# Kernel tuning notes

Hardware: AMD Instinct MI355X
Metric: run time of the kernel (lower is better)

Reference implementation:

```python
import jax, jax.numpy as jnp
import numpy as np

N_NODES = 100000
N_EDGES = 1600000
D_IN = 128
D_HID = 128
D_OUT = 64


def setup_inputs() -> dict:
    key = jax.random.key(0)
    ks = jax.random.split(key, 8)
    x = jax.random.normal(ks[0], (N_NODES, D_IN), dtype=jnp.float32)
    edge_index = jax.random.randint(ks[1], (2, N_EDGES), 0, N_NODES, dtype=jnp.int64)
    s1 = 1.0 / np.sqrt(D_IN)
    s2 = 1.0 / np.sqrt(D_HID)
    W1 = jax.random.uniform(ks[2], (D_IN, D_HID), jnp.float32, -s1, s1)
    b1 = jnp.zeros((D_HID,), jnp.float32)
    W2 = jax.random.uniform(ks[3], (D_HID, D_HID), jnp.float32, -s2, s2)
    b2 = jnp.zeros((D_HID,), jnp.float32)
    fc_W = jax.random.uniform(ks[4], (D_HID, D_OUT), jnp.float32, -s2, s2)
    fc_b = jax.random.uniform(ks[5], (D_OUT,), jnp.float32, -s2, s2)
    return {"x": x, "edge_index": edge_index, "W1": W1, "b1": b1,
            "W2": W2, "b2": b2, "fc_W": fc_W, "fc_b": fc_b}


def _gcn_norm(edge_index, n_nodes):
    # add self-loops, compute symmetric normalization D^{-1/2} A D^{-1/2}
    loops = jnp.arange(n_nodes, dtype=edge_index.dtype)
    src = jnp.concatenate([edge_index[0], loops])  # [E+N]
    dst = jnp.concatenate([edge_index[1], loops])
    ones = jnp.ones(src.shape[0], jnp.float32)
    deg = jax.ops.segment_sum(ones, dst, num_segments=n_nodes)  # [N]
    dinv = 1.0 / jnp.sqrt(deg)  # deg >= 1 thanks to self-loops
    norm = dinv[src] * dinv[dst]  # [E+N]
    return src, dst, norm


def _gcn_conv(x, W, b, src, dst, norm, n_nodes):
    h = x @ W                                  # [N, d]
    msg = h[src] * norm[:, None]               # gather + scale, [E+N, d]
    out = jax.ops.segment_sum(msg, dst, num_segments=n_nodes)  # scatter-add
    return out + b


def reference(x, edge_index, W1, b1, W2, b2, fc_W, fc_b):
    n = x.shape[0]
    src, dst, norm = _gcn_norm(edge_index, n)
    h = jax.nn.relu(_gcn_conv(x, W1, b1, src, dst, norm, n))
    # dropout is identity in inference mode
    h = jax.nn.relu(_gcn_conv(h, W2, b2, src, dst, norm, n))
    return h @ fc_W + fc_b
```

## Files before the change

kernel.cpp:

```cpp
#include <hip/hip_runtime.h>

typedef __attribute__((ext_vector_type(8))) short bf16x8;
typedef __attribute__((ext_vector_type(4))) float f32x4;
typedef __attribute__((ext_vector_type(2))) float f32x2;

__device__ __forceinline__ unsigned short f2bf(float x) {
  union { float f; unsigned u; } v; v.f = x;
  return (unsigned short)((v.u + 0x7fffu + ((v.u >> 16) & 1u)) >> 16);
}


__global__ __launch_bounds__(256) void bhist_k(const int* __restrict__ dst,
                                               int* __restrict__ bcnt, int E, int B) {
  __shared__ int h[512];
  for (int i = threadIdx.x; i < B; i += 256) h[i] = 0;
  __syncthreads();
  for (int e = blockIdx.x * 256 + threadIdx.x; e < E; e += gridDim.x * 256)
    atomicAdd(&h[dst[e] >> 8], 1);
  __syncthreads();
  for (int i = threadIdx.x; i < B; i += 256)
    if (h[i]) atomicAdd(&bcnt[i * 16], h[i]);
}

__global__ __launch_bounds__(256) void bin_k(const int* __restrict__ src,
                                             const int* __restrict__ dst,
                                             const int* __restrict__ bcnt,
                                             int* __restrict__ bfill,
                                             unsigned* __restrict__ ebuf, int E, int B) {
  __shared__ int hist[512];
  __shared__ int base[512];
  __shared__ int sd[256];
  int t = threadIdx.x;
  int i0 = 2 * t, i1 = 2 * t + 1;
  int v0 = (i0 < B) ? bcnt[i0 * 16] : 0;
  int v1 = (i1 < B) ? bcnt[i1 * 16] : 0;
  int ts = v0 + v1;
  sd[t] = ts; __syncthreads();
  for (int off = 1; off < 256; off <<= 1) {
    int x = (t >= off) ? sd[t - off] : 0;
    __syncthreads();
    sd[t] += x;
    __syncthreads();
  }
  int excl = sd[t] - ts;
  base[i0] = excl;
  base[i1] = excl + v0;
  __syncthreads();

  int chunk = (E + gridDim.x - 1) / gridDim.x;
  int e0 = blockIdx.x * chunk;
  int e1 = e0 + chunk; if (e1 > E) e1 = E;
  for (int i = t; i < B; i += 256) hist[i] = 0;
  __syncthreads();
  for (int e = e0 + t; e < e1; e += 256) atomicAdd(&hist[dst[e] >> 8], 1);
  __syncthreads();
  for (int i = t; i < B; i += 256) {
    int c = hist[i];
    hist[i] = base[i] + (c ? atomicAdd(&bfill[i * 16], c) : 0);
  }
  __syncthreads();
  for (int e = e0 + t; e < e1; e += 256) {
    int d = dst[e];
    int b = d >> 8;
    int pos = atomicAdd(&hist[b], 1);
    ebuf[pos] = ((unsigned)(d & 255) << 17) | (unsigned)src[e];
  }
}

__global__ __launch_bounds__(256) void bsort_k(const unsigned* __restrict__ ebuf,
                                               const int* __restrict__ bcnt,
                                               int* __restrict__ csr,
                                               int* __restrict__ row_start,
                                               float* __restrict__ dinv, int N, int B, int E) {
  __shared__ int cnt[256];
  __shared__ int sd[256];
  __shared__ int ofs[256];
  __shared__ int sorted[8192];
  __shared__ int s_bs, s_m;
  int b = blockIdx.x, t = threadIdx.x;
  int i0 = 2 * t, i1 = 2 * t + 1;
  int v0 = (i0 < B) ? bcnt[i0 * 16] : 0;
  int v1 = (i1 < B) ? bcnt[i1 * 16] : 0;
  int ts = v0 + v1;
  sd[t] = ts; __syncthreads();
  for (int off = 1; off < 256; off <<= 1) {
    int x = (t >= off) ? sd[t - off] : 0;
    __syncthreads();
    sd[t] += x;
    __syncthreads();
  }
  int excl = sd[t] - ts;
  if (i0 == b) { s_bs = excl; s_m = v0; }
  if (i1 == b) { s_bs = excl + v0; s_m = v1; }
  if (b == 0 && t == 0) row_start[N] = E;
  __syncthreads();
  int bs = s_bs, m = s_m;
  if (m > 8192) m = 8192;

  cnt[t] = 0;
  __syncthreads();
  for (int i = t; i < m; i += 256) atomicAdd(&cnt[ebuf[bs + i] >> 17], 1);
  __syncthreads();
  int deg = cnt[t];
  sd[t] = deg; __syncthreads();
  for (int off = 1; off < 256; off <<= 1) {
    int x = (t >= off) ? sd[t - off] : 0;
    __syncthreads();
    sd[t] += x;
    __syncthreads();
  }
  int nexcl = sd[t] - deg;
  ofs[t] = nexcl;
  int node = (b << 8) + t;
  if (node < N) {
    row_start[node] = bs + nexcl;
    dinv[node] = rsqrtf((float)(deg + 1));
  }
  __syncthreads();
  for (int i = t; i < m; i += 256) {
    unsigned r = ebuf[bs + i];
    int d = r >> 17;
    int p = atomicAdd(&ofs[d], 1);
    if (p < 8192) sorted[p] = (int)(r & 0x1FFFFu);
  }
  __syncthreads();
  for (int i = t; i < m; i += 256) csr[bs + i] = sorted[i];
}

template <int NCOL, bool INF32, bool OUTF32, bool SCALE>
__global__ __launch_bounds__(256) void gemm_k(const void* __restrict__ Ap,
                                              const float* __restrict__ W,
                                              const float* __restrict__ bias,
                                              const float* __restrict__ rowscale,
                                              void* __restrict__ Cp, int M) {
  __shared__ __align__(16) unsigned short Ws[NCOL * 136];
  int tid = threadIdx.x;
  for (int e = tid; e < 128 * NCOL; e += 256) {
    int k = e / NCOL, n = e % NCOL;
    Ws[n * 136 + k] = f2bf(W[e]);
  }
  __syncthreads();

  int wave = tid >> 6, lane = tid & 63;
  int q = lane >> 4, r = lane & 15;
  const int NT = NCOL / 16;
  int ntile = M >> 4;
  for (int tile = blockIdx.x * 4 + wave; tile < ntile; tile += gridDim.x * 4) {
    int row = tile * 16 + r;
    bf16x8 a[4];
    if (INF32) {
      const float* A = (const float*)Ap + (size_t)row * 128 + q * 8;
#pragma unroll
      for (int kk = 0; kk < 4; kk++) {
        const float4* p = (const float4*)(A + kk * 32);
        float4 f0 = p[0], f1 = p[1];
        bf16x8 tt;
        tt[0] = (short)f2bf(f0.x); tt[1] = (short)f2bf(f0.y);
        tt[2] = (short)f2bf(f0.z); tt[3] = (short)f2bf(f0.w);
        tt[4] = (short)f2bf(f1.x); tt[5] = (short)f2bf(f1.y);
        tt[6] = (short)f2bf(f1.z); tt[7] = (short)f2bf(f1.w);
        a[kk] = tt;
      }
    } else {
      const unsigned short* A = (const unsigned short*)Ap + (size_t)row * 128 + q * 8;
#pragma unroll
      for (int kk = 0; kk < 4; kk++) a[kk] = *(const bf16x8*)(A + kk * 32);
    }
    f32x4 acc[NT];
#pragma unroll
    for (int nt = 0; nt < NT; nt++) { acc[nt][0] = 0.f; acc[nt][1] = 0.f; acc[nt][2] = 0.f; acc[nt][3] = 0.f; }
#pragma unroll
    for (int kk = 0; kk < 4; kk++) {
#pragma unroll
      for (int nt = 0; nt < NT; nt++) {
        bf16x8 bfr = *(const bf16x8*)&Ws[(nt * 16 + r) * 136 + kk * 32 + q * 8];
        acc[nt] = __builtin_amdgcn_mfma_f32_16x16x32_bf16(a[kk], bfr, acc[nt], 0, 0, 0);
      }
    }
#pragma unroll
    for (int rr = 0; rr < 4; rr++) {
      int orow = tile * 16 + q * 4 + rr;
      float rs = SCALE ? rowscale[orow] : 1.f;
#pragma unroll
      for (int nt = 0; nt < NT; nt++) {
        int ocol = nt * 16 + r;
        if (OUTF32)
          ((float*)Cp)[(size_t)orow * NCOL + ocol] = acc[nt][rr] + bias[ocol];
        else
          ((unsigned short*)Cp)[(size_t)orow * NCOL + ocol] = f2bf(acc[nt][rr] * rs);
      }
    }
  }
}

__global__ __launch_bounds__(256) void agg_k(const unsigned short* __restrict__ hs,
                                             const float* __restrict__ dinv,
                                             const int* __restrict__ row_start,
                                             const int* __restrict__ csr,
                                             const float* __restrict__ bias,
                                             unsigned short* __restrict__ out, int N) {
  int lane = threadIdx.x & 63;
  int node = (blockIdx.x * 256 + threadIdx.x) >> 6;
  if (node >= N) return;
  float di = dinv[node];
  int beg = row_start[node];
  int deg = row_start[node + 1] - beg;

  const unsigned short* colp = hs + lane * 2;

  f32x2 acc; acc[0] = 0.f; acc[1] = 0.f;

  for (int base = -1; base < deg; base += 64) {
    int idx = base + lane;
    int s = node;
    if (idx >= 0 && idx < deg) s = csr[beg + idx];
    int cntv = deg - base; if (cntv > 64) cntv = 64;
    int j = 0;
    for (; j + 16 <= cntv; j += 16) {
      unsigned u[16];
#pragma unroll
      for (int k = 0; k < 16; k++) {
        int sj = __builtin_amdgcn_readlane(s, j + k);
        u[k] = *(const unsigned*)(colp + (size_t)sj * 128);
      }
#pragma unroll
      for (int k = 0; k < 16; k++) {
        f32x2 p;
        p[0] = __uint_as_float(u[k] << 16);
        p[1] = __uint_as_float(u[k] & 0xffff0000u);
        acc += p;
      }
    }
    if (j < cntv) {
      unsigned u[16];
      float w[16];
#pragma unroll
      for (int k = 0; k < 16; k++) {
        int sj = __builtin_amdgcn_readlane(s, (j + k) & 63);
        u[k] = *(const unsigned*)(colp + (size_t)sj * 128);
        w[k] = (j + k < cntv) ? 1.f : 0.f;
      }
#pragma unroll
      for (int k = 0; k < 16; k++) {
        f32x2 p;
        p[0] = __uint_as_float(u[k] << 16);
        p[1] = __uint_as_float(u[k] & 0xffff0000u);
        f32x2 wv; wv[0] = w[k]; wv[1] = w[k];
        acc += p * wv;
      }
    }
  }

  f32x2 bv = *(const f32x2*)(bias + lane * 2);
  float v0 = acc[0] * di + bv[0];
  float v1 = acc[1] * di + bv[1];
  if (v0 < 0.f) v0 = 0.f;
  if (v1 < 0.f) v1 = 0.f;
  unsigned pk = ((unsigned)f2bf(v1) << 16) | (unsigned)f2bf(v0);
  *(unsigned*)(out + (size_t)node * 128 + lane * 2) = pk;
}

extern "C" void kernel_launch(void* const* d_in, const int* in_sizes, int n_in,
                              void* d_out, int out_size, void* d_ws, size_t ws_size,
                              hipStream_t stream) {
  const float* x  = (const float*)d_in[0];
  const int* ei   = (const int*)d_in[1];
  const float* W1 = (const float*)d_in[2];
  const float* b1 = (const float*)d_in[3];
  const float* W2 = (const float*)d_in[4];
  const float* b2 = (const float*)d_in[5];
  const float* fcW = (const float*)d_in[6];
  const float* fcb = (const float*)d_in[7];
  float* out = (float*)d_out;

  int N = in_sizes[0] / 128;
  int E = in_sizes[1] / 2;
  int B = (N + 255) >> 8;
  const int* src = ei;
  const int* dst = ei + E;

  char* w = (char*)d_ws;
  auto alloc = [&](size_t b) { char* p = w; w += (b + 255) & ~(size_t)255; return p; };
  float* dinv      = (float*)alloc((size_t)N * 4);
  int*   row_start = (int*)alloc((size_t)(N + 1) * 4);
  int*   batom     = (int*)alloc((size_t)(B + 1) * 128);
  int*   bcnt      = batom;
  int*   bfill     = batom + (size_t)(B + 1) * 16;
  unsigned* ebuf   = (unsigned*)alloc((size_t)E * 4);
  int*   csr       = (int*)alloc((size_t)E * 4);
  unsigned short* bufA = (unsigned short*)alloc((size_t)N * 128 * 2);
  unsigned short* bufB = (unsigned short*)alloc((size_t)N * 128 * 2);

  hipMemsetAsync(batom, 0, (size_t)(B + 1) * 128, stream);

  bhist_k<<<256, 256, 0, stream>>>(dst, bcnt, E, B);
  bin_k<<<256, 256, 0, stream>>>(src, dst, bcnt, bfill, ebuf, E, B);
  bsort_k<<<B, 256, 0, stream>>>(ebuf, bcnt, csr, row_start, dinv, N, B, E);

  gemm_k<128, true, false, true><<<782, 256, 0, stream>>>((const void*)x, W1, nullptr, dinv,
                                                          (void*)bufA, N);
  agg_k<<<(N + 3) / 4, 256, 0, stream>>>(bufA, dinv, row_start, csr, b1, bufB, N);
  gemm_k<128, false, false, true><<<782, 256, 0, stream>>>((const void*)bufB, W2, nullptr, dinv,
                                                           (void*)bufA, N);
  agg_k<<<(N + 3) / 4, 256, 0, stream>>>(bufA, dinv, row_start, csr, b2, bufB, N);
  gemm_k<64, false, true, false><<<782, 256, 0, stream>>>((const void*)bufB, fcW, fcb, nullptr,
                                                          (void*)out, N);
}
```

Baseline: 333.9 us.

## Store hidden features in column-sliced layout and aggregate per 16-column slice

Changes the intermediate bf16 feature buffers from row-major [N,128] to eight column slices of [N,16]. The aggregation kernel now gives each block one slice, with 8 lanes per node and 8 nodes per wave, and prefetches CSR indices in groups of 4. The aim is for each slice's gather working set (about 3.2 MB) to stay resident in L2 across scattered neighbour reads. In exchange, each neighbour read is only 32 bytes, CSR indices are re-read once per slice, and lanes idle while the wave runs to the maximum degree among its 8 nodes.

```diff
diff --git a/kernel.cpp b/kernel.cpp
--- a/kernel.cpp
+++ b/kernel.cpp
@@ -141,6 +141,7 @@
   }
   __syncthreads();
 
+  size_t M16 = (size_t)M * 16;
   int wave = tid >> 6, lane = tid & 63;
   int q = lane >> 4, r = lane & 15;
   const int NT = NCOL / 16;
@@ -162,9 +163,12 @@
         a[kk] = tt;
       }
     } else {
-      const unsigned short* A = (const unsigned short*)Ap + (size_t)row * 128 + q * 8;
-#pragma unroll
-      for (int kk = 0; kk < 4; kk++) a[kk] = *(const bf16x8*)(A + kk * 32);
+      const unsigned short* A = (const unsigned short*)Ap;
+#pragma unroll
+      for (int kk = 0; kk < 4; kk++) {
+        int d0 = q * 8 + kk * 32;
+        a[kk] = *(const bf16x8*)(A + (size_t)(d0 >> 4) * M16 + (size_t)row * 16 + (d0 & 15));
+      }
     }
     f32x4 acc[NT];
 #pragma unroll
@@ -187,7 +191,8 @@
         if (OUTF32)
           ((float*)Cp)[(size_t)orow * NCOL + ocol] = acc[nt][rr] + bias[ocol];
         else
-          ((unsigned short*)Cp)[(size_t)orow * NCOL + ocol] = f2bf(acc[nt][rr] * rs);
+          *((unsigned short*)Cp + (size_t)nt * M16 + (size_t)orow * 16 + r) =
+              f2bf(acc[nt][rr] * rs);
       }
     }
   }
@@ -199,65 +204,73 @@
                                              const int* __restrict__ csr,
                                              const float* __restrict__ bias,
                                              unsigned short* __restrict__ out, int N) {
-  int lane = threadIdx.x & 63;
-  int node = (blockIdx.x * 256 + threadIdx.x) >> 6;
-  if (node >= N) return;
-  float di = dinv[node];
-  int beg = row_start[node];
-  int deg = row_start[node + 1] - beg;
-
-  const unsigned short* colp = hs + lane * 2;
-
-  f32x2 acc; acc[0] = 0.f; acc[1] = 0.f;
-
-  for (int base = -1; base < deg; base += 64) {
-    int idx = base + lane;
-    int s = node;
-    if (idx >= 0 && idx < deg) s = csr[beg + idx];
-    int cntv = deg - base; if (cntv > 64) cntv = 64;
-    int j = 0;
-    for (; j + 16 <= cntv; j += 16) {
-      unsigned u[16];
-#pragma unroll
-      for (int k = 0; k < 16; k++) {
-        int sj = __builtin_amdgcn_readlane(s, j + k);
-        u[k] = *(const unsigned*)(colp + (size_t)sj * 128);
-      }
-#pragma unroll
-      for (int k = 0; k < 16; k++) {
-        f32x2 p;
-        p[0] = __uint_as_float(u[k] << 16);
-        p[1] = __uint_as_float(u[k] & 0xffff0000u);
-        acc += p;
-      }
-    }
-    if (j < cntv) {
-      unsigned u[16];
-      float w[16];
-#pragma unroll
-      for (int k = 0; k < 16; k++) {
-        int sj = __builtin_amdgcn_readlane(s, (j + k) & 63);
-        u[k] = *(const unsigned*)(colp + (size_t)sj * 128);
-        w[k] = (j + k < cntv) ? 1.f : 0.f;
-      }
-#pragma unroll
-      for (int k = 0; k < 16; k++) {
-        f32x2 p;
-        p[0] = __uint_as_float(u[k] << 16);
-        p[1] = __uint_as_float(u[k] & 0xffff0000u);
-        f32x2 wv; wv[0] = w[k]; wv[1] = w[k];
-        acc += p * wv;
-      }
-    }
-  }
-
-  f32x2 bv = *(const f32x2*)(bias + lane * 2);
-  float v0 = acc[0] * di + bv[0];
-  float v1 = acc[1] * di + bv[1];
-  if (v0 < 0.f) v0 = 0.f;
-  if (v1 < 0.f) v1 = 0.f;
-  unsigned pk = ((unsigned)f2bf(v1) << 16) | (unsigned)f2bf(v0);
-  *(unsigned*)(out + (size_t)node * 128 + lane * 2) = pk;
+  int tid = threadIdx.x;
+  int wid = tid >> 6, lane = tid & 63;
+  int slice = blockIdx.x & 7;
+  int g = lane >> 3, l = lane & 7;
+  int node = (blockIdx.x >> 3) * 32 + wid * 8 + g;
+  bool nv = node < N;
+  int nsafe = nv ? node : 0;
+  int beg = row_start[nsafe];
+  int deg = nv ? (row_start[nsafe + 1] - beg) : 0;
+  float di = dinv[nsafe];
+
+  size_t M16 = (size_t)N * 16;
+  const unsigned short* sb = hs + (size_t)slice * M16 + l * 2;
+
+  unsigned su = *(const unsigned*)(sb + (size_t)nsafe * 16);
+  f32x2 acc;
+  acc[0] = __uint_as_float(su << 16);
+  acc[1] = __uint_as_float(su & 0xffff0000u);
+
+  int mdeg = deg;
+  mdeg = max(mdeg, __shfl_xor(mdeg, 8));
+  mdeg = max(mdeg, __shfl_xor(mdeg, 16));
+  mdeg = max(mdeg, __shfl_xor(mdeg, 32));
+
+  int c[4];
+#pragma unroll
+  for (int k = 0; k < 4; k++) {
+    int idx = (k < deg) ? beg + k : 0;
+    c[k] = __builtin_nontemporal_load(csr + idx);
+  }
+
+  for (int j = 0; j < mdeg; j += 4) {
+    int s[4]; float w[4];
+#pragma unroll
+    for (int k = 0; k < 4; k++) {
+      s[k] = c[k];
+      w[k] = (j + k < deg) ? 1.f : 0.f;
+    }
+#pragma unroll
+    for (int k = 0; k < 4; k++) {
+      int jj = j + 4 + k;
+      int idx = (jj < deg) ? beg + jj : 0;
+      c[k] = __builtin_nontemporal_load(csr + idx);
+    }
+    unsigned u[4];
+#pragma unroll
+    for (int k = 0; k < 4; k++) u[k] = *(const unsigned*)(sb + (size_t)s[k] * 16);
+#pragma unroll
+    for (int k = 0; k < 4; k++) {
+      f32x2 p;
+      p[0] = __uint_as_float(u[k] << 16);
+      p[1] = __uint_as_float(u[k] & 0xffff0000u);
+      acc[0] += p[0] * w[k];
+      acc[1] += p[1] * w[k];
+    }
+  }
+
+  if (nv) {
+    f32x2 bv = *(const f32x2*)(bias + slice * 16 + l * 2);
+    float v0 = acc[0] * di + bv[0];
+    float v1 = acc[1] * di + bv[1];
+    if (v0 < 0.f) v0 = 0.f;
+    if (v1 < 0.f) v1 = 0.f;
+    unsigned pk = ((unsigned)f2bf(v1) << 16) | (unsigned)f2bf(v0);
+    __builtin_nontemporal_store(
+        pk, (unsigned*)(out + (size_t)slice * M16 + (size_t)node * 16 + l * 2));
+  }
 }
 
 extern "C" void kernel_launch(void* const* d_in, const int* in_sizes, int n_in,
@@ -297,12 +310,14 @@
   bin_k<<<256, 256, 0, stream>>>(src, dst, bcnt, bfill, ebuf, E, B);
   bsort_k<<<B, 256, 0, stream>>>(ebuf, bcnt, csr, row_start, dinv, N, B, E);
 
+  int aggGrid = 8 * ((N + 31) / 32);
+
   gemm_k<128, true, false, true><<<782, 256, 0, stream>>>((const void*)x, W1, nullptr, dinv,
                                                           (void*)bufA, N);
-  agg_k<<<(N + 3) / 4, 256, 0, stream>>>(bufA, dinv, row_start, csr, b1, bufB, N);
+  agg_k<<<aggGrid, 256, 0, stream>>>(bufA, dinv, row_start, csr, b1, bufB, N);
   gemm_k<128, false, false, true><<<782, 256, 0, stream>>>((const void*)bufB, W2, nullptr, dinv,
                                                            (void*)bufA, N);
-  agg_k<<<(N + 3) / 4, 256, 0, stream>>>(bufA, dinv, row_start, csr, b2, bufB, N);
+  agg_k<<<aggGrid, 256, 0, stream>>>(bufA, dinv, row_start, csr, b2, bufB, N);
   gemm_k<64, false, true, false><<<782, 256, 0, stream>>>((const void*)bufB, fcW, fcb, nullptr,
                                                           (void*)out, N);
 }
```

New measurement: 571.4 us. 1.71x slower.

## Fuse second GCN aggregation with final FC layer via LDS and MFMA

Applied to the files above, without the earlier changes.

Replaces the second aggregation kernel and the final 128x64 FC GEMM with one kernel. Each 512-thread block aggregates 128 nodes into a bf16 tile held in LDS, then multiplies it by the LDS-resident bf16 fcW using MFMA before writing fp32 output. This removes the write and re-read of the hidden buffer and one launch. In exchange, blocks are larger and use more LDS, each wave handles 16 nodes serially, and every block reconverts fcW to bf16.

```diff
diff --git a/kernel.cpp b/kernel.cpp
--- a/kernel.cpp
+++ b/kernel.cpp
@@ -260,6 +260,118 @@
   *(unsigned*)(out + (size_t)node * 128 + lane * 2) = pk;
 }
 
+__global__ __launch_bounds__(512) void aggfc_k(const unsigned short* __restrict__ hs,
+                                               const float* __restrict__ dinv,
+                                               const int* __restrict__ row_start,
+                                               const int* __restrict__ csr,
+                                               const float* __restrict__ bias,
+                                               const float* __restrict__ fcW,
+                                               const float* __restrict__ fcb,
+                                               float* __restrict__ out, int N) {
+  __shared__ __align__(16) unsigned short Ws[64 * 136];
+  __shared__ __align__(16) unsigned short At[128 * 136];
+  int tid = threadIdx.x;
+  for (int e = tid; e < 128 * 64; e += 512) {
+    int k = e / 64, n = e % 64;
+    Ws[n * 136 + k] = f2bf(fcW[e]);
+  }
+  __syncthreads();
+
+  int wid = tid >> 6, lane = tid & 63;
+  int row0 = wid * 16;
+  int node0 = blockIdx.x * 128;
+
+  const unsigned short* colp = hs + lane * 2;
+
+  for (int i = 0; i < 16; i++) {
+    int node = node0 + row0 + i;
+    bool nv = node < N;
+    int nsafe = nv ? node : 0;
+    float di = dinv[nsafe];
+    int beg = row_start[nsafe];
+    int deg = nv ? (row_start[nsafe + 1] - beg) : 0;
+
+    f32x2 acc; acc[0] = 0.f; acc[1] = 0.f;
+
+    for (int base = -1; base < deg; base += 64) {
+      int idx = base + lane;
+      int s = nsafe;
+      if (idx >= 0 && idx < deg) s = csr[beg + idx];
+      int cntv = deg - base; if (cntv > 64) cntv = 64;
+      int j = 0;
+      for (; j + 16 <= cntv; j += 16) {
+        unsigned u[16];
+#pragma unroll
+        for (int k = 0; k < 16; k++) {
+          int sj = __builtin_amdgcn_readlane(s, j + k);
+          u[k] = *(const unsigned*)(colp + (size_t)sj * 128);
+        }
+#pragma unroll
+        for (int k = 0; k < 16; k++) {
+          f32x2 p;
+          p[0] = __uint_as_float(u[k] << 16);
+          p[1] = __uint_as_float(u[k] & 0xffff0000u);
+          acc += p;
+        }
+      }
+      if (j < cntv) {
+        unsigned u[16];
+        float w[16];
+#pragma unroll
+        for (int k = 0; k < 16; k++) {
+          int sj = __builtin_amdgcn_readlane(s, (j + k) & 63);
+          u[k] = *(const unsigned*)(colp + (size_t)sj * 128);
+          w[k] = (j + k < cntv) ? 1.f : 0.f;
+        }
+#pragma unroll
+        for (int k = 0; k < 16; k++) {
+          f32x2 p;
+          p[0] = __uint_as_float(u[k] << 16);
+          p[1] = __uint_as_float(u[k] & 0xffff0000u);
+          f32x2 wv; wv[0] = w[k]; wv[1] = w[k];
+          acc += p * wv;
+        }
+      }
+    }
+
+    f32x2 bv = *(const f32x2*)(bias + lane * 2);
+    float v0 = acc[0] * di + bv[0];
+    float v1 = acc[1] * di + bv[1];
+    if (v0 < 0.f || !nv) v0 = 0.f;
+    if (v1 < 0.f || !nv) v1 = 0.f;
+    unsigned pk = ((unsigned)f2bf(v1) << 16) | (unsigned)f2bf(v0);
+    *(unsigned*)&At[(row0 + i) * 136 + lane * 2] = pk;
+  }
+
+  int q = lane >> 4, r = lane & 15;
+  bf16x8 a[4];
+#pragma unroll
+  for (int kk = 0; kk < 4; kk++)
+    a[kk] = *(const bf16x8*)&At[(row0 + r) * 136 + kk * 32 + q * 8];
+  f32x4 accC[4];
+#pragma unroll
+  for (int nt = 0; nt < 4; nt++) { accC[nt][0] = 0.f; accC[nt][1] = 0.f; accC[nt][2] = 0.f; accC[nt][3] = 0.f; }
+#pragma unroll
+  for (int kk = 0; kk < 4; kk++) {
+#pragma unroll
+    for (int nt = 0; nt < 4; nt++) {
+      bf16x8 bfr = *(const bf16x8*)&Ws[(nt * 16 + r) * 136 + kk * 32 + q * 8];
+      accC[nt] = __builtin_amdgcn_mfma_f32_16x16x32_bf16(a[kk], bfr, accC[nt], 0, 0, 0);
+    }
+  }
+#pragma unroll
+  for (int rr = 0; rr < 4; rr++) {
+    int orow = node0 + row0 + q * 4 + rr;
+    if (orow < N) {
+#pragma unroll
+      for (int nt = 0; nt < 4; nt++) {
+        int ocol = nt * 16 + r;
+        out[(size_t)orow * 64 + ocol] = accC[nt][rr] + fcb[ocol];
+      }
+    }
+  }
+}
+
 extern "C" void kernel_launch(void* const* d_in, const int* in_sizes, int n_in,
                               void* d_out, int out_size, void* d_ws, size_t ws_size,
                               hipStream_t stream) {
@@ -302,7 +414,6 @@
   agg_k<<<(N + 3) / 4, 256, 0, stream>>>(bufA, dinv, row_start, csr, b1, bufB, N);
   gemm_k<128, false, false, true><<<782, 256, 0, stream>>>((const void*)bufB, W2, nullptr, dinv,
                                                            (void*)bufA, N);
-  agg_k<<<(N + 3) / 4, 256, 0, stream>>>(bufA, dinv, row_start, csr, b2, bufB, N);
-  gemm_k<64, false, true, false><<<782, 256, 0, stream>>>((const void*)bufB, fcW, fcb, nullptr,
-                                                          (void*)out, N);
-}
+  aggfc_k<<<(N + 127) / 128, 512, 0, stream>>>(bufA, dinv, row_start, csr, b2, fcW, fcb,
+                                               out, N);
+}
```

After: 355.4 us. 1.06x slower.

## Fuse CSR build kernels and memset into one cooperative kernel with grid syncs

Applied to the files above, without the earlier changes.

Replaces the memset plus three separate CSR-construction kernels (bucket histogram, binning, per-bucket sort) with a single cooperative launch that uses grid.sync between phases. The grid size becomes B blocks (391) instead of 256 for the first two phases. The aim is to remove launch overheads and inter-kernel gaps. In exchange it adds grid-wide barrier costs, and it needs all B blocks to be co-resident, which the large shared-memory footprint (sorted[8192]) could limit.

```diff
diff --git a/kernel.cpp b/kernel.cpp
--- a/kernel.cpp
+++ b/kernel.cpp
@@ -1,4 +1,7 @@
 #include <hip/hip_runtime.h>
+#include <hip/hip_cooperative_groups.h>
+
+namespace cg = cooperative_groups;
 
 typedef __attribute__((ext_vector_type(8))) short bf16x8;
 typedef __attribute__((ext_vector_type(4))) float f32x4;
@@ -9,122 +12,127 @@
   return (unsigned short)((v.u + 0x7fffu + ((v.u >> 16) & 1u)) >> 16);
 }
 
-
-__global__ __launch_bounds__(256) void bhist_k(const int* __restrict__ dst,
-                                               int* __restrict__ bcnt, int E, int B) {
-  __shared__ int h[512];
-  for (int i = threadIdx.x; i < B; i += 256) h[i] = 0;
-  __syncthreads();
-  for (int e = blockIdx.x * 256 + threadIdx.x; e < E; e += gridDim.x * 256)
-    atomicAdd(&h[dst[e] >> 8], 1);
-  __syncthreads();
-  for (int i = threadIdx.x; i < B; i += 256)
-    if (h[i]) atomicAdd(&bcnt[i * 16], h[i]);
-}
-
-__global__ __launch_bounds__(256) void bin_k(const int* __restrict__ src,
+__global__ __launch_bounds__(256) void csr_k(const int* __restrict__ src,
                                              const int* __restrict__ dst,
-                                             const int* __restrict__ bcnt,
-                                             int* __restrict__ bfill,
-                                             unsigned* __restrict__ ebuf, int E, int B) {
+                                             int* __restrict__ batom,
+                                             unsigned* __restrict__ ebuf,
+                                             int* __restrict__ csr,
+                                             int* __restrict__ row_start,
+                                             float* __restrict__ dinv,
+                                             int N, int E, int B) {
+  cg::grid_group grid = cg::this_grid();
   __shared__ int hist[512];
   __shared__ int base[512];
-  __shared__ int sd[256];
-  int t = threadIdx.x;
-  int i0 = 2 * t, i1 = 2 * t + 1;
-  int v0 = (i0 < B) ? bcnt[i0 * 16] : 0;
-  int v1 = (i1 < B) ? bcnt[i1 * 16] : 0;
-  int ts = v0 + v1;
-  sd[t] = ts; __syncthreads();
-  for (int off = 1; off < 256; off <<= 1) {
-    int x = (t >= off) ? sd[t - off] : 0;
-    __syncthreads();
-    sd[t] += x;
-    __syncthreads();
-  }
-  int excl = sd[t] - ts;
-  base[i0] = excl;
-  base[i1] = excl + v0;
-  __syncthreads();
-
-  int chunk = (E + gridDim.x - 1) / gridDim.x;
-  int e0 = blockIdx.x * chunk;
-  int e1 = e0 + chunk; if (e1 > E) e1 = E;
-  for (int i = t; i < B; i += 256) hist[i] = 0;
-  __syncthreads();
-  for (int e = e0 + t; e < e1; e += 256) atomicAdd(&hist[dst[e] >> 8], 1);
-  __syncthreads();
-  for (int i = t; i < B; i += 256) {
-    int c = hist[i];
-    hist[i] = base[i] + (c ? atomicAdd(&bfill[i * 16], c) : 0);
-  }
-  __syncthreads();
-  for (int e = e0 + t; e < e1; e += 256) {
-    int d = dst[e];
-    int b = d >> 8;
-    int pos = atomicAdd(&hist[b], 1);
-    ebuf[pos] = ((unsigned)(d & 255) << 17) | (unsigned)src[e];
-  }
-}
-
-__global__ __launch_bounds__(256) void bsort_k(const unsigned* __restrict__ ebuf,
-                                               const int* __restrict__ bcnt,
-                                               int* __restrict__ csr,
-                                               int* __restrict__ row_start,
-                                               float* __restrict__ dinv, int N, int B, int E) {
-  __shared__ int cnt[256];
   __shared__ int sd[256];
   __shared__ int ofs[256];
   __shared__ int sorted[8192];
   __shared__ int s_bs, s_m;
-  int b = blockIdx.x, t = threadIdx.x;
-  int i0 = 2 * t, i1 = 2 * t + 1;
-  int v0 = (i0 < B) ? bcnt[i0 * 16] : 0;
-  int v1 = (i1 < B) ? bcnt[i1 * 16] : 0;
-  int ts = v0 + v1;
-  sd[t] = ts; __syncthreads();
-  for (int off = 1; off < 256; off <<= 1) {
-    int x = (t >= off) ? sd[t - off] : 0;
-    __syncthreads();
-    sd[t] += x;
-    __syncthreads();
-  }
-  int excl = sd[t] - ts;
-  if (i0 == b) { s_bs = excl; s_m = v0; }
-  if (i1 == b) { s_bs = excl + v0; s_m = v1; }
-  if (b == 0 && t == 0) row_start[N] = E;
+
+  int t = threadIdx.x;
+  int* bcnt = batom;
+  int* bfill = batom + (size_t)(B + 1) * 16;
+
+  int tot = (B + 1) * 32;
+  for (int i = blockIdx.x * 256 + t; i < tot; i += gridDim.x * 256) batom[i] = 0;
+  grid.sync();
+
+  for (int i = t; i < B; i += 256) hist[i] = 0;
   __syncthreads();
-  int bs = s_bs, m = s_m;
-  if (m > 8192) m = 8192;
-
-  cnt[t] = 0;
+  for (int e = blockIdx.x * 256 + t; e < E; e += gridDim.x * 256)
+    atomicAdd(&hist[dst[e] >> 8], 1);
   __syncthreads();
-  for (int i = t; i < m; i += 256) atomicAdd(&cnt[ebuf[bs + i] >> 17], 1);
-  __syncthreads();
-  int deg = cnt[t];
-  sd[t] = deg; __syncthreads();
-  for (int off = 1; off < 256; off <<= 1) {
-    int x = (t >= off) ? sd[t - off] : 0;
-    __syncthreads();
-    sd[t] += x;
-    __syncthreads();
-  }
-  int nexcl = sd[t] - deg;
-  ofs[t] = nexcl;
-  int node = (b << 8) + t;
-  if (node < N) {
-    row_start[node] = bs + nexcl;
-    dinv[node] = rsqrtf((float)(deg + 1));
-  }
-  __syncthreads();
-  for (int i = t; i < m; i += 256) {
-    unsigned r = ebuf[bs + i];
-    int d = r >> 17;
-    int p = atomicAdd(&ofs[d], 1);
-    if (p < 8192) sorted[p] = (int)(r & 0x1FFFFu);
-  }
-  __syncthreads();
-  for (int i = t; i < m; i += 256) csr[bs + i] = sorted[i];
+  for (int i = t; i < B; i += 256)
+    if (hist[i]) atomicAdd(&bcnt[i * 16], hist[i]);
+  grid.sync();
+
+  {
+    int i0 = 2 * t, i1 = 2 * t + 1;
+    int v0 = (i0 < B) ? bcnt[i0 * 16] : 0;
+    int v1 = (i1 < B) ? bcnt[i1 * 16] : 0;
+    int ts = v0 + v1;
+    sd[t] = ts; __syncthreads();
+    for (int off = 1; off < 256; off <<= 1) {
+      int x = (t >= off) ? sd[t - off] : 0;
+      __syncthreads();
+      sd[t] += x;
+      __syncthreads();
+    }
+    int excl = sd[t] - ts;
+    base[i0] = excl;
+    base[i1] = excl + v0;
+    __syncthreads();
+
+    int chunk = (E + gridDim.x - 1) / gridDim.x;
+    int e0 = blockIdx.x * chunk;
+    int e1 = e0 + chunk; if (e1 > E) e1 = E;
+    for (int i = t; i < B; i += 256) hist[i] = 0;
+    __syncthreads();
+    for (int e = e0 + t; e < e1; e += 256) atomicAdd(&hist[dst[e] >> 8], 1);
+    __syncthreads();
+    for (int i = t; i < B; i += 256) {
+      int c = hist[i];
+      hist[i] = base[i] + (c ? atomicAdd(&bfill[i * 16], c) : 0);
+    }
+    __syncthreads();
+    for (int e = e0 + t; e < e1; e += 256) {
+      int d = dst[e];
+      int b = d >> 8;
+      int pos = atomicAdd(&hist[b], 1);
+      ebuf[pos] = ((unsigned)(d & 255) << 17) | (unsigned)src[e];
+    }
+  }
+  grid.sync();
+
+  {
+    int b = blockIdx.x;
+    int i0 = 2 * t, i1 = 2 * t + 1;
+    int v0 = (i0 < B) ? bcnt[i0 * 16] : 0;
+    int v1 = (i1 < B) ? bcnt[i1 * 16] : 0;
+    int ts = v0 + v1;
+    sd[t] = ts; __syncthreads();
+    for (int off = 1; off < 256; off <<= 1) {
+      int x = (t >= off) ? sd[t - off] : 0;
+      __syncthreads();
+      sd[t] += x;
+      __syncthreads();
+    }
+    int excl = sd[t] - ts;
+    if (i0 == b) { s_bs = excl; s_m = v0; }
+    if (i1 == b) { s_bs = excl + v0; s_m = v1; }
+    if (b == 0 && t == 0) row_start[N] = E;
+    __syncthreads();
+    int bs = s_bs, m = s_m;
+    if (m > 8192) m = 8192;
+
+    hist[t] = 0;
+    __syncthreads();
+    for (int i = t; i < m; i += 256) atomicAdd(&hist[ebuf[bs + i] >> 17], 1);
+    __syncthreads();
+    int deg = hist[t];
+    sd[t] = deg; __syncthreads();
+    for (int off = 1; off < 256; off <<= 1) {
+      int x = (t >= off) ? sd[t - off] : 0;
+      __syncthreads();
+      sd[t] += x;
+      __syncthreads();
+    }
+    int nexcl = sd[t] - deg;
+    ofs[t] = nexcl;
+    int node = (b << 8) + t;
+    if (node < N) {
+      row_start[node] = bs + nexcl;
+      dinv[node] = rsqrtf((float)(deg + 1));
+    }
+    __syncthreads();
+    for (int i = t; i < m; i += 256) {
+      unsigned r = ebuf[bs + i];
+      int d = r >> 17;
+      int p = atomicAdd(&ofs[d], 1);
+      if (p < 8192) sorted[p] = (int)(r & 0x1FFFFu);
+    }
+    __syncthreads();
+    for (int i = t; i < m; i += 256) csr[bs + i] = sorted[i];
+  }
 }
 
 template <int NCOL, bool INF32, bool OUTF32, bool SCALE>
@@ -284,18 +292,17 @@
   float* dinv      = (float*)alloc((size_t)N * 4);
   int*   row_start = (int*)alloc((size_t)(N + 1) * 4);
   int*   batom     = (int*)alloc((size_t)(B + 1) * 128);
-  int*   bcnt      = batom;
-  int*   bfill     = batom + (size_t)(B + 1) * 16;
   unsigned* ebuf   = (unsigned*)alloc((size_t)E * 4);
   int*   csr       = (int*)alloc((size_t)E * 4);
   unsigned short* bufA = (unsigned short*)alloc((size_t)N * 128 * 2);
   unsigned short* bufB = (unsigned short*)alloc((size_t)N * 128 * 2);
 
-  hipMemsetAsync(batom, 0, (size_t)(B + 1) * 128, stream);
-
-  bhist_k<<<256, 256, 0, stream>>>(dst, bcnt, E, B);
-  bin_k<<<256, 256, 0, stream>>>(src, dst, bcnt, bfill, ebuf, E, B);
-  bsort_k<<<B, 256, 0, stream>>>(ebuf, bcnt, csr, row_start, dinv, N, B, E);
+  {
+    void* args[] = {(void*)&src, (void*)&dst, (void*)&batom, (void*)&ebuf,
+                    (void*)&csr, (void*)&row_start, (void*)&dinv,
+                    (void*)&N, (void*)&E, (void*)&B};
+    hipLaunchCooperativeKernel((const void*)csr_k, dim3(B), dim3(256), args, 0, stream);
+  }
 
   gemm_k<128, true, false, true><<<782, 256, 0, stream>>>((const void*)x, W1, nullptr, dinv,
                                                           (void*)bufA, N);
```

Measured after the change: 484.7 us. +45.1%, slower.
